# Optimization experiments

Measured on AMD Instinct MI355X. Metric: run time of the kernel, lower is better.

## Reference

```python
import jax, jax.numpy as jnp
import numpy as np

GROUPS = 32
EPS = 1e-5


def setup_inputs() -> dict:
    key = jax.random.key(0)
    ks = jax.random.split(key, 4)
    b, c, h, w = 4, 256, 64, 64
    x = jax.random.normal(ks[0], (b, c, h, w), dtype=jnp.float32)
    gn_gamma = jnp.ones((c,), dtype=jnp.float32)
    gn_beta = jnp.zeros((c,), dtype=jnp.float32)
    # 1x1 convs are pointwise linear maps: store kernels as [out, in]
    w_qkv = jax.random.normal(ks[1], (3 * c, c), dtype=jnp.float32) * (1.0 / np.sqrt(c))
    b_qkv = jnp.zeros((3 * c,), dtype=jnp.float32)
    w_out = jax.random.normal(ks[2], (c, c), dtype=jnp.float32) * (1.0 / np.sqrt(c))
    b_out = jnp.zeros((c,), dtype=jnp.float32)
    return {"x": x, "gn_gamma": gn_gamma, "gn_beta": gn_beta,
            "w_qkv": w_qkv, "b_qkv": b_qkv, "w_out": w_out, "b_out": b_out}


def reference(x, gn_gamma, gn_beta, w_qkv, b_qkv, w_out, b_out):
    b, c, h, w = x.shape
    # GroupNorm(32, c)
    xg = x.reshape(b, GROUPS, c // GROUPS, h, w)
    mean = jnp.mean(xg, axis=(2, 3, 4), keepdims=True)
    var = jnp.var(xg, axis=(2, 3, 4), keepdims=True)
    xn = ((xg - mean) * jax.lax.rsqrt(var + EPS)).reshape(b, c, h, w)
    xn = xn * gn_gamma[None, :, None, None] + gn_beta[None, :, None, None]
    # 1x1 conv QKV projection: [b, 3c, h, w]
    qkv = jnp.einsum('bchw,oc->bohw', xn, w_qkv) + b_qkv[None, :, None, None]
    q, k, v = jnp.split(qkv, 3, axis=1)
    n = h * w
    q = q.transpose(0, 2, 3, 1).reshape(b, n, c)  # [b, n, c]
    k = k.reshape(b, c, n)                        # [b, c, n]
    v = v.transpose(0, 2, 3, 1).reshape(b, n, c)  # [b, n, c]
    scores = jnp.einsum('bic,bcj->bij', q, k) * (c ** -0.5)  # [b, n, n]
    attn = jax.nn.softmax(scores, axis=-1)
    out = jnp.einsum('bij,bjc->bic', attn, v)     # [b, n, c]
    out = out.reshape(b, h, w, c).transpose(0, 3, 1, 2)  # [b, c, h, w]
    out = jnp.einsum('bchw,oc->bohw', out, w_out) + b_out[None, :, None, None]
    return out + x
```

## Files before the change

kernel.cpp:

```cpp
#include <hip/hip_runtime.h>
#include <hip/hip_bf16.h>
#include <cstdint>
#include <cstddef>

#define DEVINL __device__ __forceinline__

typedef unsigned short u16;
typedef unsigned char u8;
typedef unsigned int u32;
typedef unsigned long long u64;
typedef __attribute__((ext_vector_type(8))) short short8;
typedef __attribute__((ext_vector_type(4))) float f32x4;
typedef __attribute__((ext_vector_type(4))) u32 u32x4;

constexpr int CH = 256;
constexpr int HW = 4096;
constexpr int NB = 4;
constexpr float M0L = 5.7707801636f;
constexpr float QKS = 0.3002805f;

DEVINL u16 f2bf(float f) {
  union { float f; u32 u; } v; v.f = f;
  u32 u = v.u;
  u32 r = u + 0x7FFFu + ((u >> 16) & 1u);
  return (u16)(r >> 16);
}
DEVINL float bf2f(u16 h) {
  union { u32 u; float f; } v; v.u = ((u32)h) << 16; return v.f;
}
DEVINL float fexp2(float x) {
  float r; asm("v_exp_f32 %0, %1" : "=v"(r) : "v"(x)); return r;
}
DEVINL u8 f2fp8(float v) {
  return (u8)(__builtin_amdgcn_cvt_pk_fp8_f32(v, v, 0, false) & 0xFF);
}
DEVINL u32 pk4fp8(float v0, float v1, float v2, float v3) {
  int r = __builtin_amdgcn_cvt_pk_fp8_f32(v0, v1, 0, false);
  r = __builtin_amdgcn_cvt_pk_fp8_f32(v2, v3, r, true);
  return (u32)r;
}
DEVINL void plswap(u32& a, u32& b) {
  asm("v_permlane32_swap_b32 %0, %1" : "+v"(a), "+v"(b));
  asm("v_permlane16_swap_b32 %0, %1" : "+v"(a), "+v"(b));
}

DEVINL void gl_lds16(const void* g, void* l) {
  __builtin_amdgcn_global_load_lds(
      (__attribute__((address_space(1))) void*)(size_t)g,
      (__attribute__((address_space(3))) void*)l, 16, 0, 0);
}

DEVINL f32x4 mfma_bf16(short8 a, short8 b, f32x4 c) {
  return __builtin_amdgcn_mfma_f32_16x16x32_bf16(a, b, c, 0, 0, 0);
}
DEVINL f32x4 mfma_fp8(long a, long b, f32x4 c) {
  return __builtin_amdgcn_mfma_f32_16x16x32_fp8_fp8(a, b, c, 0, 0, 0);
}


__global__ void k_pre(const float* __restrict__ x, float* __restrict__ stats,
                      const float* __restrict__ wq, const float* __restrict__ wo,
                      u8* __restrict__ w38, u16* __restrict__ wobP) {
  if (blockIdx.x >= 128) {
    int i = (blockIdx.x - 128) * 256 + threadIdx.x;
    w38[i] = f2fp8(wq[i]);
    if (i < 65536) {
      int o = i >> 8, pc = i & 255;
      wobP[i] = f2bf(wo[o * 256 + ((pc & 15) * 16 + (pc >> 4))]);
    }
    return;
  }
  int bg = blockIdx.x;
  const float* p = x + (size_t)bg * 32768;
  float s = 0.f, ss = 0.f;
  for (int i = threadIdx.x; i < 8192; i += 256) {
    float4 v = ((const float4*)p)[i];
    s += v.x + v.y + v.z + v.w;
    ss += v.x * v.x + v.y * v.y + v.z * v.z + v.w * v.w;
  }
  for (int m = 32; m; m >>= 1) { s += __shfl_xor(s, m); ss += __shfl_xor(ss, m); }
  __shared__ float rs[4], rss[4];
  int w = threadIdx.x >> 6;
  if ((threadIdx.x & 63) == 0) { rs[w] = s; rss[w] = ss; }
  __syncthreads();
  if (threadIdx.x == 0) {
    s = rs[0] + rs[1] + rs[2] + rs[3];
    ss = rss[0] + rss[1] + rss[2] + rss[3];
    float mean = s / 32768.f;
    float var = ss / 32768.f - mean * mean;
    stats[bg * 2] = mean;
    stats[bg * 2 + 1] = rsqrtf(var + 1e-5f);
  }
}

__global__ void k_norm(const float* __restrict__ x, const float* __restrict__ stats,
                       const float* __restrict__ gamma, const float* __restrict__ beta,
                       u8* __restrict__ xn8) {
  int bid = blockIdx.x;
  int b = bid >> 8, ct = (bid >> 6) & 3, pt = bid & 63;
  int c0 = ct * 64, p0 = pt * 64;
  __shared__ u16 tile[64][66];
  const float* xb = x + ((size_t)b * CH + c0) * HW + p0;
#pragma unroll
  for (int it = 0; it < 4; it++) {
    int li = threadIdx.x + it * 256;
    int ci = li >> 4, pq = (li & 15) * 4;
    float4 v = *(const float4*)(xb + (size_t)ci * HW + pq);
    int c = c0 + ci;
    int gg = c >> 3;
    float mean = stats[(b * 32 + gg) * 2], rstd = stats[(b * 32 + gg) * 2 + 1];
    float ga = gamma[c] * rstd;
    float be = beta[c] - mean * ga;
    tile[ci][pq + 0] = f2bf(v.x * ga + be);
    tile[ci][pq + 1] = f2bf(v.y * ga + be);
    tile[ci][pq + 2] = f2bf(v.z * ga + be);
    tile[ci][pq + 3] = f2bf(v.w * ga + be);
  }
  __syncthreads();
#pragma unroll
  for (int it = 0; it < 2; it++) {
    int ch = threadIdx.x + it * 256;
    int pr = ch >> 3, cc = (ch & 7) * 8;
    float v[8];
#pragma unroll
    for (int q2 = 0; q2 < 8; q2++) v[q2] = bf2f(tile[cc + q2][pr]);
    u32 lo = pk4fp8(v[0], v[1], v[2], v[3]);
    u32 hi = pk4fp8(v[4], v[5], v[6], v[7]);
    *(u64*)(xn8 + ((size_t)b * HW + p0 + pr) * CH + c0 + cc) = ((u64)hi << 32) | lo;
  }
}

DEVINL short8 ldsA(const char* base, int row, int colb) {
  return *(const short8*)(base + row * 128 + (colb ^ ((row & 7) << 4)));
}

__global__ __launch_bounds__(256, 2) void k_qkv(
    const u8* __restrict__ xn8, const u8* __restrict__ w38,
    const float* __restrict__ bqkv,
    u8* __restrict__ Qg8, u8* __restrict__ Kg8, u8* __restrict__ Vg8) {
  int bid = blockIdx.x;
  int b = bid / 192; int rm = bid - b * 192; int mt = rm / 6, nt = rm - mt * 6;
  extern __shared__ char sm[];
  const int tid = threadIdx.x, w = tid >> 6, lane = tid & 63, t = lane & 15, g = lane >> 4;
  const u8* Abase = xn8 + ((size_t)b * HW + mt * 128) * CH;
  const u8* Bbase = w38 + (size_t)nt * 128 * CH;
  f32x4 acc[4][4] = {};

  auto stg = [&](char* dst, const u8* src, int kt) {
#pragma unroll
    for (int it = 0; it < 2; it++) {
      int CI = w * 128 + it * 64 + lane;
      int row = CI >> 2, c4 = CI & 3;
      int sc = c4 ^ ((row ^ (row >> 2)) & 3);
      gl_lds16(src + (size_t)row * CH + kt * 64 + sc * 16, dst + w * 2048 + it * 1024);
    }
  };

  stg(sm, Abase, 0);
  stg(sm + 16384, Bbase, 0);
  __syncthreads();
  for (int kt = 0; kt < 4; kt++) {
    int cur = kt & 1;
    if (kt < 3) {
      stg(sm + ((cur ^ 1) * 8192), Abase, kt + 1);
      stg(sm + 16384 + ((cur ^ 1) * 8192), Bbase, kt + 1);
    }
    const char* Asm = sm + cur * 8192;
    const char* Bsm = sm + 16384 + cur * 8192;
#pragma unroll
    for (int ks = 0; ks < 2; ks++) {
      long af[4], bf4[4];
#pragma unroll
      for (int m = 0; m < 4; m++) {
        int r = 64 * (w >> 1) + 16 * m + t;
        af[m] = *(const long*)(Asm + r * 64 +
                 (((ks * 2 + (g >> 1)) ^ ((r ^ (r >> 2)) & 3)) << 4) + ((g & 1) << 3));
      }
#pragma unroll
      for (int n = 0; n < 4; n++) {
        int r = 64 * (w & 1) + 16 * n + t;
        bf4[n] = *(const long*)(Bsm + r * 64 +
                 (((ks * 2 + (g >> 1)) ^ ((r ^ (r >> 2)) & 3)) << 4) + ((g & 1) << 3));
      }
#pragma unroll
      for (int m = 0; m < 4; m++)
#pragma unroll
        for (int n = 0; n < 4; n++)
          acc[m][n] = mfma_fp8(af[m], bf4[n], acc[m][n]);
    }
    __syncthreads();
  }
  if (nt < 4) {
    u8* dst = (nt < 2) ? Qg8 : Kg8;
    int pcb = t * 16 + (nt & 1) * 8 + 4 * (w & 1);
    float bias[4];
#pragma unroll
    for (int n = 0; n < 4; n++) bias[n] = bqkv[nt * 128 + 64 * (w & 1) + 16 * n + t];
#pragma unroll
    for (int m = 0; m < 4; m++) {
      int p0 = mt * 128 + 64 * (w >> 1) + 16 * m + 4 * g;
#pragma unroll
      for (int rr = 0; rr < 4; rr++) {
        u32 word = pk4fp8((acc[m][0][rr] + bias[0]) * QKS,
                          (acc[m][1][rr] + bias[1]) * QKS,
                          (acc[m][2][rr] + bias[2]) * QKS,
                          (acc[m][3][rr] + bias[3]) * QKS);
        *(u32*)(dst + ((size_t)b * HW + p0 + rr) * CH + pcb) = word;
      }
    }
  } else {
#pragma unroll
    for (int n = 0; n < 4; n++) {
      int o = nt * 128 + 64 * (w & 1) + 16 * n + t;
      float bias = bqkv[o];
      int oo = o - 512;
#pragma unroll
      for (int m = 0; m < 4; m++) {
        int p0 = mt * 128 + 64 * (w >> 1) + 16 * m + 4 * g;
        u32 pv = pk4fp8(acc[m][n][0] + bias, acc[m][n][1] + bias,
                        acc[m][n][2] + bias, acc[m][n][3] + bias);
        *(u32*)(Vg8 + (size_t)b * CH * HW + (size_t)oo * HW + p0) = pv;
      }
    }
  }
}

__global__ __launch_bounds__(512, 2) void k_attn(
    const u8* __restrict__ Qg8, const u8* __restrict__ Kg8, const u8* __restrict__ Vg8,
    u8* __restrict__ Op8, float* __restrict__ ml) {
  int bid = blockIdx.x;
  int qb = bid >> 4, b = (bid >> 2) & 3, split = bid & 3;
  extern __shared__ char sm[];
  const int tid = threadIdx.x, w = tid >> 6, lane = tid & 63, t = lane & 15, g = lane >> 4;
  const u8* Qb = Qg8 + (size_t)b * HW * CH;
  const u8* Kb = Kg8 + (size_t)b * HW * CH;
  const u8* Vb = Vg8 + (size_t)b * CH * HW;
  int qrow0 = qb * 256 + w * 32;
  int kv0 = split * 1024;

  long q8[2][8];
#pragma unroll
  for (int rf = 0; rf < 2; rf++)
#pragma unroll
    for (int ks = 0; ks < 8; ks++)
      q8[rf][ks] = *(const long*)(Qb + (size_t)(qrow0 + rf * 16 + t) * CH + ks * 32 + g * 8);

  f32x4 oacc[2][16] = {};
  float lsum[2] = {0.f, 0.f};
  f32x4 sf[2][4];
  long pf[2][2];

  int kOffB[2], vOffB[2];
#pragma unroll
  for (int it = 0; it < 2; it++) {
    int CI = w * 128 + it * 64 + lane;
    int row = CI >> 4, c = CI & 15;
    kOffB[it] = row * 256 + ((c ^ (row & 7)) * 16);
    int rv = CI >> 2, c4 = CI & 3;
    vOffB[it] = rv * HW + ((c4 ^ ((rv >> 1) & 3)) * 16);
  }
  auto stageKV = [&](int kbuf, int vbuf, int tt) {
    char* KL = sm + kbuf * 16384 + w * 2048;
    char* VL = sm + 49152 + vbuf * 16384 + w * 2048;
    const u8* ksrc = Kb + (size_t)(kv0 + tt * 64) * CH;
    const u8* vsrc = Vb + (kv0 + tt * 64);
#pragma unroll
    for (int it = 0; it < 2; it++) gl_lds16(ksrc + kOffB[it], KL + it * 1024);
#pragma unroll
    for (int it = 0; it < 2; it++) gl_lds16(vsrc + vOffB[it], VL + it * 1024);
  };

  auto QK = [&](const char* KL) {
#pragma unroll
    for (int jf = 0; jf < 4; jf++) {
      int row = jf * 16 + t;
      f32x4 a0 = {}, a1 = {};
#pragma unroll
      for (int ks = 0; ks < 8; ks++) {
        int s = ks * 4 + g;
        long kf = *(const long*)(KL + row * 256 + (((s >> 1) ^ (row & 7)) << 4) + ((s & 1) << 3));
        a0 = mfma_fp8(kf, q8[0][ks], a0);
        a1 = mfma_fp8(kf, q8[1][ks], a1);
      }
      sf[0][jf] = a0; sf[1][jf] = a1;
    }
  };
  auto PV = [&](const char* VL) {
#pragma unroll
    for (int ks = 0; ks < 2; ks++)
#pragma unroll
      for (int cf = 0; cf < 16; cf++) {
        int row = cf * 16 + t;
        long vf = *(const long*)(VL + row * 64 +
                    (((ks * 2 + (g >> 1)) ^ ((row >> 1) & 3)) << 4) + ((g & 1) << 3));
        oacc[0][cf] = mfma_fp8(pf[0][ks], vf, oacc[0][cf]);
        oacc[1][cf] = mfma_fp8(pf[1][ks], vf, oacc[1][cf]);
      }
  };
  auto SM = [&]() {
#pragma unroll
    for (int rf = 0; rf < 2; rf++) {
      u32 A4[4];
#pragma unroll
      for (int jf = 0; jf < 4; jf++) {
        float e0 = fexp2(sf[rf][jf][0] - M0L);
        float e1 = fexp2(sf[rf][jf][1] - M0L);
        float e2 = fexp2(sf[rf][jf][2] - M0L);
        float e3 = fexp2(sf[rf][jf][3] - M0L);
        lsum[rf] += (e0 + e1) + (e2 + e3);
        A4[jf] = pk4fp8(e0, e1, e2, e3);
      }
#pragma unroll
      for (int ks = 0; ks < 2; ks++) {
        u32 X = A4[2 * ks], Y = A4[2 * ks + 1];
        plswap(X, Y);
        pf[rf][ks] = (long)(((u64)Y << 32) | X);
      }
    }
  };

  stageKV(0, 0, 0);
  stageKV(1, 1, 1);
  asm volatile("s_waitcnt vmcnt(4)" ::: "memory");
  __builtin_amdgcn_s_barrier();
  __builtin_amdgcn_sched_barrier(0);
  __builtin_amdgcn_s_setprio(1);
  QK(sm + 0);
  __builtin_amdgcn_s_setprio(0);
  SM();

  for (int tt = 1; tt < 16; tt++) {
    int kcur = tt % 3, vprv = (tt - 1) & 3;
    stageKV((tt + 1) % 3, (tt + 1) & 3, (tt + 1) & 15);
    asm volatile("s_waitcnt vmcnt(4)" ::: "memory");
    __builtin_amdgcn_s_barrier();
    __builtin_amdgcn_sched_barrier(0);
    __builtin_amdgcn_s_setprio(1);
    PV(sm + 49152 + vprv * 16384);
    QK(sm + kcur * 16384);
    __builtin_amdgcn_s_setprio(0);
    SM();
  }
  __builtin_amdgcn_s_setprio(1);
  PV(sm + 49152 + 3 * 16384);
  __builtin_amdgcn_s_setprio(0);

  size_t obase = (size_t)(split * NB + b) * HW;
#pragma unroll
  for (int rf = 0; rf < 2; rf++) {
    float ls = lsum[rf];
    ls += __shfl_xor(ls, 16);
    ls += __shfl_xor(ls, 32);
    if (g == 0) ml[obase + qrow0 + rf * 16 + t] = ls;
    float invr[4];
#pragma unroll
    for (int rr = 0; rr < 4; rr++) invr[rr] = 1.f / __shfl(ls, 4 * g + rr);
#pragma unroll
    for (int rr = 0; rr < 4; rr++) {
      int row = qrow0 + rf * 16 + 4 * g + rr;
      u32x4 wv;
#pragma unroll
      for (int q4 = 0; q4 < 4; q4++)
        wv[q4] = pk4fp8(oacc[rf][4 * q4 + 0][rr] * invr[rr],
                        oacc[rf][4 * q4 + 1][rr] * invr[rr],
                        oacc[rf][4 * q4 + 2][rr] * invr[rr],
                        oacc[rf][4 * q4 + 3][rr] * invr[rr]);
      *(u32x4*)(Op8 + (obase + row) * CH + t * 16) = wv;
    }
  }
}

__global__ __launch_bounds__(256, 1) void k_oproj(
    const u16* __restrict__ wobP, const u8* __restrict__ Op8, const float* __restrict__ ml,
    const float* __restrict__ bout, const float* __restrict__ x,
    float* __restrict__ out) {
  int bid = blockIdx.x;
  int b = bid >> 6, pt = bid & 63;
  extern __shared__ char sm[];
  const int tid = threadIdx.x, w = tid >> 6, lane = tid & 63, t = lane & 15, g = lane >> 4;

  auto stageA = [&](char* dst, int kt) {
#pragma unroll
    for (int it = 0; it < 8; it++) {
      int CI = w * 512 + it * 64 + lane;
      int row = CI >> 3, ci = CI & 7;
      int sci = ci ^ (row & 7);
      gl_lds16(wobP + (size_t)row * CH + kt * 64 + sci * 8,
               dst + w * 8192 + it * 1024);
    }
  };
  auto stageB = [&](char* dst, int kt) {
#pragma unroll
    for (int it = 0; it < 2; it++) {
      int CI = w * 128 + it * 64 + lane;
      int row = CI >> 3, ci = CI & 7;
      int sci = ci ^ (row & 7);
      int p = pt * 64 + row;
      float l = 0.f;
      float accv[8] = {};
#pragma unroll
      for (int s = 0; s < 4; s++) {
        size_t r = (size_t)(s * NB + b) * HW + p;
        float lsv = ml[r];
        l += lsv;
        u64 a8 = *(const u64*)(Op8 + r * CH + kt * 64 + sci * 8);
        u32 wlo = (u32)a8, whi = (u32)(a8 >> 32);
        accv[0] += lsv * __builtin_amdgcn_cvt_f32_fp8(wlo, 0);
        accv[1] += lsv * __builtin_amdgcn_cvt_f32_fp8(wlo, 1);
        accv[2] += lsv * __builtin_amdgcn_cvt_f32_fp8(wlo, 2);
        accv[3] += lsv * __builtin_amdgcn_cvt_f32_fp8(wlo, 3);
        accv[4] += lsv * __builtin_amdgcn_cvt_f32_fp8(whi, 0);
        accv[5] += lsv * __builtin_amdgcn_cvt_f32_fp8(whi, 1);
        accv[6] += lsv * __builtin_amdgcn_cvt_f32_fp8(whi, 2);
        accv[7] += lsv * __builtin_amdgcn_cvt_f32_fp8(whi, 3);
      }
      float inv = 1.f / l;
      short8 res;
#pragma unroll
      for (int q2 = 0; q2 < 8; q2++) res[q2] = (short)f2bf(accv[q2] * inv);
      *(short8*)(dst + CI * 16) = res;
    }
  };

  f32x4 acc[4][4] = {};
  stageA(sm, 0);
  stageB(sm + 65536, 0);
  __syncthreads();
  for (int kt = 0; kt < 4; kt++) {
    int cur = kt & 1;
    if (kt < 3) {
      stageA(sm + ((cur ^ 1) * 32768), kt + 1);
      stageB(sm + 65536 + ((cur ^ 1) * 8192), kt + 1);
    }
    const char* Asm = sm + cur * 32768;
    const char* Bsm = sm + 65536 + cur * 8192;
#pragma unroll
    for (int ks = 0; ks < 2; ks++) {
      short8 af[4], bf[4];
#pragma unroll
      for (int m = 0; m < 4; m++) af[m] = ldsA(Asm, w * 64 + 16 * m + t, ks * 64 + g * 16);
#pragma unroll
      for (int n = 0; n < 4; n++) bf[n] = ldsA(Bsm, 16 * n + t, ks * 64 + g * 16);
#pragma unroll
      for (int m = 0; m < 4; m++)
#pragma unroll
        for (int n = 0; n < 4; n++)
          acc[m][n] = mfma_bf16(af[m], bf[n], acc[m][n]);
    }
    __syncthreads();
  }
#pragma unroll
  for (int m = 0; m < 4; m++) {
    int o0 = w * 64 + 16 * m + 4 * g;
#pragma unroll
    for (int n = 0; n < 4; n++) {
      int p = pt * 64 + 16 * n + t;
#pragma unroll
      for (int rr = 0; rr < 4; rr++) {
        int o = o0 + rr;
        size_t off = ((size_t)b * CH + o) * HW + p;
        out[off] = acc[m][n][rr] + bout[o] + x[off];
      }
    }
  }
}

extern "C" void kernel_launch(void* const* d_in, const int* in_sizes, int n_in,
                              void* d_out, int out_size, void* d_ws, size_t ws_size,
                              hipStream_t stream) {
  const float* x = (const float*)d_in[0];
  const float* gamma = (const float*)d_in[1];
  const float* beta = (const float*)d_in[2];
  const float* wqkv = (const float*)d_in[3];
  const float* bqkv = (const float*)d_in[4];
  const float* wout = (const float*)d_in[5];
  const float* bout = (const float*)d_in[6];
  float* out = (float*)d_out;
  char* ws = (char*)d_ws;

  float* stats = (float*)(ws);
  u8* w38 = (u8*)(ws + 1024);
  u16* wobP = (u16*)(ws + 1024 + 196608);
  u8* xn8 = (u8*)(ws + 1024 + 196608 + 131072);
  u8* Qg8 = (u8*)(ws + 328704 + 1ull * 4194304);
  u8* Kg8 = (u8*)(ws + 328704 + 2ull * 4194304);
  u8* Vg8 = (u8*)(ws + 328704 + 3ull * 4194304);
  u8* Op8 = (u8*)(ws + 328704 + 4ull * 4194304);
  float* ml = (float*)(ws + 328704 + 8ull * 4194304);

  hipFuncSetAttribute(reinterpret_cast<const void*>(k_qkv),
                      hipFuncAttributeMaxDynamicSharedMemorySize, 32768);
  hipFuncSetAttribute(reinterpret_cast<const void*>(k_oproj),
                      hipFuncAttributeMaxDynamicSharedMemorySize, 81920);
  hipFuncSetAttribute(reinterpret_cast<const void*>(k_attn),
                      hipFuncAttributeMaxDynamicSharedMemorySize, 114688);

  k_pre<<<896, 256, 0, stream>>>(x, stats, wqkv, wout, w38, wobP);
  k_norm<<<1024, 256, 0, stream>>>(x, stats, gamma, beta, xn8);
  k_qkv<<<768, 256, 32768, stream>>>(xn8, w38, bqkv, Qg8, Kg8, Vg8);
  k_attn<<<256, 512, 114688, stream>>>(Qg8, Kg8, Vg8, Op8, ml);
  k_oproj<<<256, 256, 81920, stream>>>(wobP, Op8, ml, bout, x, out);
}
```

Before: 99.81 us.

## Permute Q/K/V fp8 layouts so attention loads 16-byte fragments

Reorders the fp8 Q, K and V layouts written by the projection kernel. Each lane now holds adjacent k-slices contiguously, so the attention kernel's QK and PV loops issue one 16-byte LDS/global read per two MFMAs instead of two 8-byte reads. The aim is to halve LDS read instruction count and address arithmetic in the inner loops. Correctness depends on the projection write permutation matching the consumer's k-index mapping, and the dot product is invariant to a consistent k permutation across operands. The PV side also depends on how P's fragments line up with the permuted V.

```diff
diff --git a/kernel.cpp b/kernel.cpp
--- a/kernel.cpp
+++ b/kernel.cpp
@@ -12,6 +12,7 @@
 typedef __attribute__((ext_vector_type(8))) short short8;
 typedef __attribute__((ext_vector_type(4))) float f32x4;
 typedef __attribute__((ext_vector_type(4))) u32 u32x4;
+typedef __attribute__((ext_vector_type(2))) long long2v;
 
 constexpr int CH = 256;
 constexpr int HW = 4096;
@@ -192,7 +193,7 @@
   }
   if (nt < 4) {
     u8* dst = (nt < 2) ? Qg8 : Kg8;
-    int pcb = t * 16 + (nt & 1) * 8 + 4 * (w & 1);
+    int pcb = (t >> 2) * 64 + (t & 1) * 32 + (nt & 1) * 16 + ((t >> 1) & 1) * 8 + (w & 1) * 4;
     float bias[4];
 #pragma unroll
     for (int n = 0; n < 4; n++) bias[n] = bqkv[nt * 128 + 64 * (w & 1) + 16 * n + t];
@@ -216,10 +217,11 @@
       int oo = o - 512;
 #pragma unroll
       for (int m = 0; m < 4; m++) {
-        int p0 = mt * 128 + 64 * (w >> 1) + 16 * m + 4 * g;
+        int b4p = (g & 1) + ((m >> 1) & 1) * 2 + (g >> 1) * 4 + (m & 1) * 8;
+        int p = mt * 128 + 64 * (w >> 1) + b4p * 4;
         u32 pv = pk4fp8(acc[m][n][0] + bias, acc[m][n][1] + bias,
                         acc[m][n][2] + bias, acc[m][n][3] + bias);
-        *(u32*)(Vg8 + (size_t)b * CH * HW + (size_t)oo * HW + p0) = pv;
+        *(u32*)(Vg8 + (size_t)b * CH * HW + (size_t)oo * HW + p) = pv;
       }
     }
   }
@@ -238,12 +240,12 @@
   int qrow0 = qb * 256 + w * 32;
   int kv0 = split * 1024;
 
-  long q8[2][8];
+  long2v q16[2][4];
 #pragma unroll
   for (int rf = 0; rf < 2; rf++)
 #pragma unroll
-    for (int ks = 0; ks < 8; ks++)
-      q8[rf][ks] = *(const long*)(Qb + (size_t)(qrow0 + rf * 16 + t) * CH + ks * 32 + g * 8);
+    for (int kp = 0; kp < 4; kp++)
+      q16[rf][kp] = *(const long2v*)(Qb + (size_t)(qrow0 + rf * 16 + t) * CH + kp * 64 + g * 16);
 
   f32x4 oacc[2][16] = {};
   float lsum[2] = {0.f, 0.f};
@@ -276,26 +278,28 @@
       int row = jf * 16 + t;
       f32x4 a0 = {}, a1 = {};
 #pragma unroll
-      for (int ks = 0; ks < 8; ks++) {
-        int s = ks * 4 + g;
-        long kf = *(const long*)(KL + row * 256 + (((s >> 1) ^ (row & 7)) << 4) + ((s & 1) << 3));
-        a0 = mfma_fp8(kf, q8[0][ks], a0);
-        a1 = mfma_fp8(kf, q8[1][ks], a1);
+      for (int kp = 0; kp < 4; kp++) {
+        int q = (kp * 4 + g) ^ (row & 7);
+        long2v kf = *(const long2v*)(KL + row * 256 + q * 16);
+        a0 = mfma_fp8(kf[0], q16[0][kp][0], a0);
+        a1 = mfma_fp8(kf[0], q16[1][kp][0], a1);
+        a0 = mfma_fp8(kf[1], q16[0][kp][1], a0);
+        a1 = mfma_fp8(kf[1], q16[1][kp][1], a1);
       }
       sf[0][jf] = a0; sf[1][jf] = a1;
     }
   };
   auto PV = [&](const char* VL) {
 #pragma unroll
-    for (int ks = 0; ks < 2; ks++)
-#pragma unroll
-      for (int cf = 0; cf < 16; cf++) {
-        int row = cf * 16 + t;
-        long vf = *(const long*)(VL + row * 64 +
-                    (((ks * 2 + (g >> 1)) ^ ((row >> 1) & 3)) << 4) + ((g & 1) << 3));
-        oacc[0][cf] = mfma_fp8(pf[0][ks], vf, oacc[0][cf]);
-        oacc[1][cf] = mfma_fp8(pf[1][ks], vf, oacc[1][cf]);
-      }
+    for (int cf = 0; cf < 16; cf++) {
+      int row = cf * 16 + t;
+      int q = g ^ ((row >> 1) & 3);
+      long2v vf = *(const long2v*)(VL + row * 64 + q * 16);
+      oacc[0][cf] = mfma_fp8(pf[0][0], vf[0], oacc[0][cf]);
+      oacc[1][cf] = mfma_fp8(pf[1][0], vf[0], oacc[1][cf]);
+      oacc[0][cf] = mfma_fp8(pf[0][1], vf[1], oacc[0][cf]);
+      oacc[1][cf] = mfma_fp8(pf[1][1], vf[1], oacc[1][cf]);
+    }
   };
   auto SM = [&]() {
 #pragma unroll
```

Result: faster. 95.20 us, median of 2 (-4.6%).
